# Performance work log

Hardware: AMD Instinct MI355X
Metric: run time of the kernel (lower is better)

The kernel has to match this reference:

```python
import jax, jax.numpy as jnp
import numpy as np

D_MODEL = 1024
NUM_HEADS = 16
D_K = D_MODEL // NUM_HEADS
THETA = 10000.0
BATCH = 2
SEQ = 2048


def apply_rope(x, token_positions):
    # x: [B, H, S, D_K]; token_positions: [S] int
    half = D_K // 2
    inv_freq = THETA ** (-(jnp.arange(half, dtype=jnp.float32) * 2.0) / D_K)  # [half]
    angles = token_positions.astype(jnp.float32)[:, None] * inv_freq[None, :]  # [S, half]
    cos = jnp.cos(angles)  # [S, half]
    sin = jnp.sin(angles)
    x1 = x[..., 0::2]  # even indices
    x2 = x[..., 1::2]  # odd indices
    out_even = x1 * cos - x2 * sin
    out_odd = x1 * sin + x2 * cos
    # interleave back: [..., S, half, 2] -> [..., S, D_K]
    return jnp.stack([out_even, out_odd], axis=-1).reshape(x.shape)


def setup_inputs() -> dict:
    key = jax.random.key(0)
    ks = jax.random.split(key, 5)
    x = jax.random.normal(ks[0], (BATCH, SEQ, D_MODEL), dtype=jnp.float32)
    token_positions = jnp.arange(SEQ, dtype=jnp.int64)
    scale = 0.02
    Wq = jax.random.normal(ks[1], (D_MODEL, D_MODEL), dtype=jnp.float32) * scale
    Wk = jax.random.normal(ks[2], (D_MODEL, D_MODEL), dtype=jnp.float32) * scale
    Wv = jax.random.normal(ks[3], (D_MODEL, D_MODEL), dtype=jnp.float32) * scale
    Wo = jax.random.normal(ks[4], (D_MODEL, D_MODEL), dtype=jnp.float32) * scale
    return {"x": x, "token_positions": token_positions, "Wq": Wq, "Wk": Wk, "Wv": Wv, "Wo": Wo}


def reference(x, token_positions, Wq, Wk, Wv, Wo):
    B, S, _ = x.shape
    # cs336 Linear: y = x @ W.T with W of shape (out, in), no bias
    def proj(W):
        h = jnp.einsum('bsd,od->bso', x, W)
        return h.reshape(B, S, NUM_HEADS, D_K).transpose(0, 2, 1, 3)  # [B,H,S,Dk]
    Q = apply_rope(proj(Wq), token_positions)
    K = apply_rope(proj(Wk), token_positions)
    V = proj(Wv)
    scores = jnp.einsum('bhqd,bhkd->bhqk', Q, K) / jnp.sqrt(jnp.float32(D_K))
    causal = jnp.tril(jnp.ones((S, S), dtype=bool))
    scores = jnp.where(causal, scores, -jnp.inf)
    attn = jax.nn.softmax(scores, axis=-1)
    out = jnp.einsum('bhqk,bhkd->bhqd', attn, V)  # [B,H,S,Dk]
    out = out.transpose(0, 2, 1, 3).reshape(B, S, D_MODEL)
    return jnp.einsum('bsd,od->bso', out, Wo)
```

## Files before the change

kernel.cpp:

```cpp
#include <hip/hip_runtime.h>
#include <hip/hip_bf16.h>
#include <math.h>

#define NHEADS 16
#define DKH 64
#define SEQ 2048
#define DMODEL 1024

typedef __attribute__((ext_vector_type(8))) short short8;
typedef __attribute__((ext_vector_type(4))) float f32x4;

#define GLDS16(g, l)                                         \
  __builtin_amdgcn_global_load_lds(                          \
      (__attribute__((address_space(1))) void*)(void*)(g),   \
      (__attribute__((address_space(3))) void*)(l), 16, 0, 0)

__device__ __forceinline__ short f2bf(float f) {
  unsigned u = __float_as_uint(f);
  unsigned r = (u + 0x7fffu + ((u >> 16) & 1u)) >> 16;
  return (short)r;
}

__device__ __forceinline__ short8 pack8(float4 a, float4 b) {
  short8 v;
  v[0] = f2bf(a.x); v[1] = f2bf(a.y); v[2] = f2bf(a.z); v[3] = f2bf(a.w);
  v[4] = f2bf(b.x); v[5] = f2bf(b.y); v[6] = f2bf(b.z); v[7] = f2bf(b.w);
  return v;
}

__device__ __forceinline__ int swz(int r, int gran) {
  return r * 64 + ((gran ^ (r & 7)) << 3);
}

__global__ __launch_bounds__(256) void precast_rope_kernel(
    const float* __restrict__ X, const float* __restrict__ Wq,
    const float* __restrict__ Wk, const float* __restrict__ Wv,
    const float* __restrict__ Wo, const int* __restrict__ tp,
    short* __restrict__ Xb, short* __restrict__ Wqb, short* __restrict__ Wkb,
    short* __restrict__ Wvb, short* __restrict__ Wob,
    float* __restrict__ ct, float* __restrict__ st) {
  int bid = blockIdx.x;
  if (bid < 4096) {
    int i = bid * 256 + threadIdx.x;
    const float* src; short* dst; int off;
    if (i < 524288) { src = X; dst = Xb; off = i; }
    else {
      int k = i - 524288; int w = k >> 17; off = k & 131071;
      src = (w == 0) ? Wq : (w == 1) ? Wk : (w == 2) ? Wv : Wo;
      dst = (w == 0) ? Wqb : (w == 1) ? Wkb : (w == 2) ? Wvb : Wob;
    }
    const float4* p = reinterpret_cast<const float4*>(src) + 2 * (size_t)off;
    float4 a = p[0], b = p[1];
    reinterpret_cast<short8*>(dst)[off] = pack8(a, b);
  } else {
    int idx = (bid - 4096) * 256 + threadIdx.x;
    if (idx >= SEQ * 32) return;
    int s = idx >> 5, i = idx & 31;
    int is64 = (tp[1] == 0);
    int p = is64 ? tp[2 * s] : tp[s];
    float invf = powf(10000.0f, -(2.0f * (float)i) / 64.0f);
    float a = (float)p * invf;
    ct[idx] = cosf(a);
    st[idx] = sinf(a);
  }
}

__global__ __launch_bounds__(512, 2) void gemm_qkv_kernel(
    const short* __restrict__ X, const short* __restrict__ Wq,
    const short* __restrict__ Wk, const short* __restrict__ Wv,
    short* __restrict__ Qb, short* __restrict__ Kb, short* __restrict__ Vb,
    const float* __restrict__ ct, const float* __restrict__ st) {
  __shared__ __align__(16) short As[2][256 * 64];
  __shared__ __align__(16) short Bs[2][192 * 64];
  const int id = blockIdx.x;
  const int xcd = id & 7, rr = id >> 3;
  const int tm = (xcd & 3) * 4 + (rr & 3);
  const int tn = (xcd >> 2) * 8 + (rr >> 2);
  const int tid = threadIdx.x;
  const int wave = tid >> 6, lane = tid & 63;
  const int l15 = lane & 15, quad = lane >> 4;
  const int wm = wave >> 2, wn = wave & 3;

  const int n0 = tn * 192;
  const short* Abase = X + (size_t)(tm * 256) * DMODEL;
  const short* Bbase = Wq + (size_t)n0 * DMODEL;
  (void)Wk; (void)Wv;

  const int lr = lane >> 3;
  const int lc = (lane & 7) ^ lr;

#define STGA(bufi, half, kt_)                                              \
  do {                                                                     \
    int R0 = (half) * 128 + wave * 16;                                     \
    GLDS16(Abase + (size_t)(R0 + lr) * DMODEL + (kt_) * 64 + lc * 8,       \
           &As[bufi][R0 * 64 + lane * 8]);                                 \
    GLDS16(Abase + (size_t)(R0 + 8 + lr) * DMODEL + (kt_) * 64 + lc * 8,   \
           &As[bufi][(R0 + 8) * 64 + lane * 8]);                           \
  } while (0)
#define STGB(bufi, t, kt_)                                                 \
  do {                                                                     \
    int R0 = (t) * 64 + wave * 8;                                          \
    GLDS16(Bbase + (size_t)(R0 + lr) * DMODEL + (kt_) * 64 + lc * 8,       \
           &Bs[bufi][R0 * 64 + lane * 8]);                                 \
  } while (0)

  f32x4 acc[8][3];
#pragma unroll
  for (int m = 0; m < 8; m++)
#pragma unroll
    for (int n = 0; n < 3; n++) acc[m][n] = (f32x4){0.f, 0.f, 0.f, 0.f};

  STGB(0, 0, 0); STGB(0, 1, 0); STGB(0, 2, 0);
  STGA(0, 0, 0); STGA(0, 1, 0);
  STGB(1, 0, 1); STGB(1, 1, 1); STGB(1, 2, 1);

  short8 bfr[3][2];
  for (int kt = 0; kt < 16; kt++) {
    const int buf = kt & 1;
    if (kt < 15) { STGA(buf ^ 1, 0, kt + 1); }
    if (kt < 15) { asm volatile("s_waitcnt vmcnt(5)" ::: "memory"); }
    else         { asm volatile("s_waitcnt vmcnt(0)" ::: "memory"); }
    asm volatile("s_barrier" ::: "memory");
#pragma unroll
    for (int nb = 0; nb < 3; nb++)
#pragma unroll
      for (int ks = 0; ks < 2; ks++)
        bfr[nb][ks] = *reinterpret_cast<const short8*>(
            &Bs[buf][swz(wn * 48 + nb * 16 + l15, ks * 4 + quad)]);
    {
      short8 af[2][2];
#pragma unroll
      for (int j = 0; j < 2; j++)
#pragma unroll
        for (int ks = 0; ks < 2; ks++)
          af[j][ks] = *reinterpret_cast<const short8*>(
              &As[buf][swz(wm * 128 + j * 16 + l15, ks * 4 + quad)]);
      __builtin_amdgcn_s_setprio(1);
#pragma unroll
      for (int j = 0; j < 2; j++)
#pragma unroll
        for (int nb = 0; nb < 3; nb++)
#pragma unroll
          for (int ks = 0; ks < 2; ks++)
            acc[j][nb] = __builtin_amdgcn_mfma_f32_16x16x32_bf16(
                af[j][ks], bfr[nb][ks], acc[j][nb], 0, 0, 0);
      __builtin_amdgcn_s_setprio(0);
    }
    asm volatile("s_barrier" ::: "memory");
#pragma unroll
    for (int p = 1; p < 4; p++) {
      short8 af[2][2];
#pragma unroll
      for (int j = 0; j < 2; j++)
#pragma unroll
        for (int ks = 0; ks < 2; ks++)
          af[j][ks] = *reinterpret_cast<const short8*>(
              &As[buf][swz(wm * 128 + (p * 2 + j) * 16 + l15, ks * 4 + quad)]);
      if (p == 1)      { if (kt < 15) { STGA(buf ^ 1, 1, kt + 1); } }
      else if (p == 2) { if (kt < 14) { STGB(buf, 0, kt + 2); STGB(buf, 1, kt + 2); } }
      else             { if (kt < 14) { STGB(buf, 2, kt + 2); } }
      asm volatile("s_barrier" ::: "memory");
      __builtin_amdgcn_s_setprio(1);
#pragma unroll
      for (int j = 0; j < 2; j++)
#pragma unroll
        for (int nb = 0; nb < 3; nb++)
#pragma unroll
          for (int ks = 0; ks < 2; ks++)
            acc[p * 2 + j][nb] = __builtin_amdgcn_mfma_f32_16x16x32_bf16(
                af[j][ks], bfr[nb][ks], acc[p * 2 + j][nb], 0, 0, 0);
      __builtin_amdgcn_s_setprio(0);
      asm volatile("s_barrier" ::: "memory");
    }
  }
#undef STGA
#undef STGB

#pragma unroll
  for (int mf = 0; mf < 8; mf++) {
    const int s0g = tm * 256 + wm * 128 + mf * 16 + quad * 4;
    const int b = s0g >> 11, s = s0g & 2047;
#pragma unroll
    for (int nb = 0; nb < 3; nb++) {
      int nl = n0 + wn * 48 + nb * 16 + l15;
      int mid = nl >> 10;
      int c = nl & 1023;
      int h = c >> 6, dd = c & 63;
      if (mid == 2) {
        unsigned u0 = (unsigned)(unsigned short)f2bf(acc[mf][nb][0]) |
                      ((unsigned)(unsigned short)f2bf(acc[mf][nb][1]) << 16);
        unsigned u1 = (unsigned)(unsigned short)f2bf(acc[mf][nb][2]) |
                      ((unsigned)(unsigned short)f2bf(acc[mf][nb][3]) << 16);
        uint2 pk; pk.x = u0; pk.y = u1;
        *reinterpret_cast<uint2*>(Vb + ((size_t)(b * NHEADS + h) * DKH + dd) * SEQ + s) = pk;
      } else {
#pragma unroll
        for (int reg = 0; reg < 4; reg++) {
          float v = acc[mf][nb][reg];
          float pv = __shfl_xor(v, 1);
          int fi = dd >> 1;
          int sg = s + reg;
          float cc = ct[sg * 32 + fi], sn = st[sg * 32 + fi];
          float o = (dd & 1) ? (pv * sn + v * cc) : (v * cc - pv * sn);
          size_t oi = (((size_t)(b * NHEADS + h)) * SEQ + sg) * DKH + dd;
          ((mid == 0) ? Qb : Kb)[oi] = f2bf(o);
        }
      }
    }
  }
}

__global__ __launch_bounds__(256, 4) void attn_kernel(
    const short* __restrict__ Qb, const short* __restrict__ Kb,
    const short* __restrict__ Vtb, short* __restrict__ Ob) {
  __shared__ __align__(16) short QPs[64 * 64];
  __shared__ __align__(16) short Ks[2][64 * 64];
  __shared__ __align__(16) short Vs[2][64 * 64];

  const int id = blockIdx.x;
  const int xx = id & 7;
  const int mm = (((id >> 3) & 3) + (id >> 8)) & 3;
  const int bh = id >> 5;
  const int qt = (mm == 0) ? (31 - xx) : (mm == 1) ? (16 + xx)
               : (mm == 2) ? (15 - xx) : xx;

  const int tid = threadIdx.x;
  const int wave = tid >> 6, lane = tid & 63;
  const int l15 = lane & 15, quad = lane >> 4;
  const int sr0 = tid >> 3, sc = tid & 7;

  const short* Qp = Qb + (size_t)bh * SEQ * DKH;
  const short* Kp = Kb + (size_t)bh * SEQ * DKH;
  const short* Vp = Vtb + (size_t)bh * DKH * SEQ;

  uint4 kreg[2], vreg[2];
#pragma unroll
  for (int i = 0; i < 2; i++) {
    int r = sr0 + i * 32;
    kreg[i] = *reinterpret_cast<const uint4*>(Kp + (size_t)r * DKH + sc * 8);
    vreg[i] = *reinterpret_cast<const uint4*>(Vp + (size_t)r * SEQ + sc * 8);
  }
#pragma unroll
  for (int i = 0; i < 2; i++) {
    int r = sr0 + i * 32;
    uint4 v = *reinterpret_cast<const uint4*>(Qp + (size_t)(qt * 64 + r) * DKH + sc * 8);
    *reinterpret_cast<uint4*>(&QPs[swz(r, sc)]) = v;
  }
#pragma unroll
  for (int i = 0; i < 2; i++) {
    int r = sr0 + i * 32;
    *reinterpret_cast<uint4*>(&Ks[0][swz(r, sc)]) = kreg[i];
    *reinterpret_cast<uint4*>(&Vs[0][swz(r, sc)]) = vreg[i];
  }
  __syncthreads();
  short8 qf0, qf1;
  {
    int r = wave * 16 + l15;
    qf0 = *reinterpret_cast<const short8*>(&QPs[swz(r, quad)]);
    qf1 = *reinterpret_cast<const short8*>(&QPs[swz(r, 4 + quad)]);
  }

  f32x4 accO[4];
#pragma unroll
  for (int i = 0; i < 4; i++) accO[i] = (f32x4){0.f, 0.f, 0.f, 0.f};
  float rs = 0.f;

  const float SCL = 0.125f * 1.44269504089f;
  const float FM = 13.0f;

  int buf = 0;
  for (int kt = 0; kt <= qt; kt++) {
    if (kt < qt) {
#pragma unroll
      for (int i = 0; i < 2; i++) {
        int r = sr0 + i * 32;
        kreg[i] = *reinterpret_cast<const uint4*>(Kp + (size_t)((kt + 1) * 64 + r) * DKH + sc * 8);
        vreg[i] = *reinterpret_cast<const uint4*>(Vp + (size_t)r * SEQ + (kt + 1) * 64 + sc * 8);
      }
    }

    f32x4 sa[4];
#pragma unroll
    for (int nb = 0; nb < 4; nb++) {
      sa[nb] = (f32x4){0.f, 0.f, 0.f, 0.f};
      int r = nb * 16 + l15;
      short8 kf0 = *reinterpret_cast<const short8*>(&Ks[buf][swz(r, quad)]);
      sa[nb] = __builtin_amdgcn_mfma_f32_16x16x32_bf16(kf0, qf0, sa[nb], 0, 0, 0);
      short8 kf1 = *reinterpret_cast<const short8*>(&Ks[buf][swz(r, 4 + quad)]);
      sa[nb] = __builtin_amdgcn_mfma_f32_16x16x32_bf16(kf1, qf1, sa[nb], 0, 0, 0);
    }

    const bool diag = (kt == qt);
    const int prow = wave * 16 + l15;
#pragma unroll
    for (int nb = 0; nb < 4; nb++) {
      float p0 = exp2f(sa[nb][0] * SCL - FM);
      float p1 = exp2f(sa[nb][1] * SCL - FM);
      float p2 = exp2f(sa[nb][2] * SCL - FM);
      float p3 = exp2f(sa[nb][3] * SCL - FM);
      if (diag) {
        int kbase = nb * 16 + quad * 4;
        if (kbase + 0 > prow) p0 = 0.f;
        if (kbase + 1 > prow) p1 = 0.f;
        if (kbase + 2 > prow) p2 = 0.f;
        if (kbase + 3 > prow) p3 = 0.f;
      }
      rs += (p0 + p1) + (p2 + p3);
      unsigned u0 = (unsigned)(unsigned short)f2bf(p0) |
                    ((unsigned)(unsigned short)f2bf(p1) << 16);
      unsigned u1 = (unsigned)(unsigned short)f2bf(p2) |
                    ((unsigned)(unsigned short)f2bf(p3) << 16);
      uint2 pk; pk.x = u0; pk.y = u1;
      int g = 2 * nb + (quad >> 1);
      *reinterpret_cast<uint2*>(&QPs[swz(prow, g) + (quad & 1) * 4]) = pk;
    }

    short8 pf0 = *reinterpret_cast<const short8*>(&QPs[swz(prow, quad)]);
    short8 pf1 = *reinterpret_cast<const short8*>(&QPs[swz(prow, 4 + quad)]);
#pragma unroll
    for (int db = 0; db < 4; db++) {
      int dv = db * 16 + l15;
      short8 vf0 = *reinterpret_cast<const short8*>(&Vs[buf][swz(dv, quad)]);
      accO[db] = __builtin_amdgcn_mfma_f32_16x16x32_bf16(pf0, vf0, accO[db], 0, 0, 0);
      short8 vf1 = *reinterpret_cast<const short8*>(&Vs[buf][swz(dv, 4 + quad)]);
      accO[db] = __builtin_amdgcn_mfma_f32_16x16x32_bf16(pf1, vf1, accO[db], 0, 0, 0);
    }

    if (kt < qt) {
      int nbuf = buf ^ 1;
#pragma unroll
      for (int i = 0; i < 2; i++) {
        int r = sr0 + i * 32;
        *reinterpret_cast<uint4*>(&Ks[nbuf][swz(r, sc)]) = kreg[i];
        *reinterpret_cast<uint4*>(&Vs[nbuf][swz(r, sc)]) = vreg[i];
      }
      __syncthreads();
      buf = nbuf;
    }
  }

  float t = rs;
  t += __shfl_xor(t, 16);
  t += __shfl_xor(t, 32);
  float lv[4];
#pragma unroll
  for (int reg = 0; reg < 4; reg++) lv[reg] = __shfl(t, quad * 4 + reg);

  int b = bh >> 4, h = bh & 15;
#pragma unroll
  for (int db = 0; db < 4; db++)
#pragma unroll
    for (int reg = 0; reg < 4; reg++) {
      int s = qt * 64 + wave * 16 + quad * 4 + reg;
      int dv = db * 16 + l15;
      float o = accO[db][reg] / lv[reg];
      Ob[((size_t)(b * SEQ + s)) * DMODEL + h * DKH + dv] = f2bf(o);
    }
}

__global__ __launch_bounds__(256) void gemm_out_kernel(
    const short* __restrict__ X, const short* __restrict__ Wo, float* __restrict__ Out) {
  __shared__ __align__(16) short As[128 * 64];
  __shared__ __align__(16) short Bs[64 * 64];
  const int tm = blockIdx.x;
  const int tn = blockIdx.y;
  const int tid = threadIdx.x;
  const int wave = tid >> 6, lane = tid & 63;
  const int l15 = lane & 15, quad = lane >> 4;
  const int wm = wave >> 1, wn = wave & 1;

  const short* Abase = X + (size_t)(tm * 128) * DMODEL;
  const short* Bbase = Wo + (size_t)(tn * 64) * DMODEL;

  const int lr = lane >> 3;
  const int lc = (lane & 7) ^ lr;

  f32x4 acc[4][2];
#pragma unroll
  for (int mb = 0; mb < 4; mb++)
#pragma unroll
    for (int nb = 0; nb < 2; nb++) acc[mb][nb] = (f32x4){0.f, 0.f, 0.f, 0.f};

  for (int kk = 0; kk < 16; kk++) {
    const short* Ak = Abase + kk * 64;
    const short* Bk = Bbase + kk * 64;
#pragma unroll
    for (int i = 0; i < 4; i++) {
      int R = i * 32 + wave * 8;
      GLDS16(Ak + (size_t)(R + lr) * DMODEL + lc * 8, &As[R * 64 + lane * 8]);
    }
#pragma unroll
    for (int i = 0; i < 2; i++) {
      int R = i * 32 + wave * 8;
      GLDS16(Bk + (size_t)(R + lr) * DMODEL + lc * 8, &Bs[R * 64 + lane * 8]);
    }
    __syncthreads();
#pragma unroll
    for (int kg = 0; kg < 2; kg++) {
      short8 af[4], bf[2];
#pragma unroll
      for (int mb = 0; mb < 4; mb++) {
        int r = wm * 64 + mb * 16 + l15;
        af[mb] = *reinterpret_cast<const short8*>(&As[swz(r, kg * 4 + quad)]);
      }
#pragma unroll
      for (int nb = 0; nb < 2; nb++) {
        int r = wn * 32 + nb * 16 + l15;
        bf[nb] = *reinterpret_cast<const short8*>(&Bs[swz(r, kg * 4 + quad)]);
      }
#pragma unroll
      for (int mb = 0; mb < 4; mb++)
#pragma unroll
        for (int nb = 0; nb < 2; nb++)
          acc[mb][nb] = __builtin_amdgcn_mfma_f32_16x16x32_bf16(af[mb], bf[nb], acc[mb][nb], 0, 0, 0);
    }
    __syncthreads();
  }
#pragma unroll
  for (int mb = 0; mb < 4; mb++)
#pragma unroll
    for (int nb = 0; nb < 2; nb++)
#pragma unroll
      for (int reg = 0; reg < 4; reg++) {
        int rg = tm * 128 + wm * 64 + mb * 16 + quad * 4 + reg;
        int col = tn * 64 + wn * 32 + nb * 16 + l15;
        Out[(size_t)rg * DMODEL + col] = acc[mb][nb][reg];
      }
}

extern "C" void kernel_launch(void* const* d_in, const int* in_sizes, int n_in,
                              void* d_out, int out_size, void* d_ws, size_t ws_size,
                              hipStream_t stream) {
  (void)in_sizes; (void)n_in; (void)out_size; (void)ws_size;
  const float* X  = (const float*)d_in[0];
  const int*   tp = (const int*)d_in[1];
  const float* Wq = (const float*)d_in[2];
  const float* Wk = (const float*)d_in[3];
  const float* Wv = (const float*)d_in[4];
  const float* Wo = (const float*)d_in[5];
  float* Out = (float*)d_out;

  short* Qb  = (short*)d_ws;
  short* Kb  = Qb + 4194304;
  short* Vb  = Kb + 4194304;
  short* Ab  = Vb + 4194304;
  short* Xb  = Ab + 4194304;
  short* Wqb = Xb + 4194304;
  short* Wkb = Wqb + 1048576;
  short* Wvb = Wkb + 1048576;
  short* Wob = Wvb + 1048576;
  float* ct  = (float*)(Wob + 1048576);
  float* st  = ct + SEQ * 32;

  precast_rope_kernel<<<dim3(4352), dim3(256), 0, stream>>>(
      X, Wq, Wk, Wv, Wo, tp, Xb, Wqb, Wkb, Wvb, Wob, ct, st);
  gemm_qkv_kernel<<<dim3(256), dim3(512), 0, stream>>>(Xb, Wqb, Wkb, Wvb,
                                                       Qb, Kb, Vb, ct, st);
  attn_kernel<<<dim3(1024), dim3(256), 0, stream>>>(Qb, Kb, Vb, Ab);
  gemm_out_kernel<<<dim3(32, 16), dim3(256), 0, stream>>>(Ab, Wob, Out);
}
```

Before: 183.1 us.

## Remap attention blocks, add MFMA priority hints and hardware bf16 packing

Changes the block-to-(batch-head, q-tile) mapping so that consecutive block groups pair short and long causal q-tiles (u and 31-u) and spread batch-heads across XCD-strided ids. This is meant to balance work per CU and improve L2 locality. It also wraps the MFMA sections in s_setprio to favour matrix issue across waves, and replaces the software bf16 rounding with the v_cvt_pk_bf16_f32 instruction. It adds a __syncthreads after the Q fragment read, so later P writes into the shared Q/P buffer cannot race with other waves still reading Q. That barrier fixes a latent hazard at the cost of one extra sync.

```diff
diff --git a/kernel.cpp b/kernel.cpp
--- a/kernel.cpp
+++ b/kernel.cpp
@@ -19,6 +19,12 @@
   unsigned u = __float_as_uint(f);
   unsigned r = (u + 0x7fffu + ((u >> 16) & 1u)) >> 16;
   return (short)r;
+}
+
+__device__ __forceinline__ unsigned cvtpk(float lo, float hi) {
+  unsigned r;
+  asm("v_cvt_pk_bf16_f32 %0, %1, %2" : "=v"(r) : "v"(lo), "v"(hi));
+  return r;
 }
 
 __device__ __forceinline__ short8 pack8(float4 a, float4 b) {
@@ -218,11 +224,11 @@
   __shared__ __align__(16) short Vs[2][64 * 64];
 
   const int id = blockIdx.x;
-  const int xx = id & 7;
-  const int mm = (((id >> 3) & 3) + (id >> 8)) & 3;
-  const int bh = id >> 5;
-  const int qt = (mm == 0) ? (31 - xx) : (mm == 1) ? (16 + xx)
-               : (mm == 2) ? (15 - xx) : xx;
+  const int x8 = id & 7;
+  const int g  = id >> 3;
+  const int bh = x8 * 4 + (g >> 5);
+  const int u  = g & 31;
+  const int qt = (u & 1) ? (31 - (u >> 1)) : (u >> 1);
 
   const int tid = threadIdx.x;
   const int wave = tid >> 6, lane = tid & 63;
@@ -259,6 +265,7 @@
     qf0 = *reinterpret_cast<const short8*>(&QPs[swz(r, quad)]);
     qf1 = *reinterpret_cast<const short8*>(&QPs[swz(r, 4 + quad)]);
   }
+  __syncthreads();
 
   f32x4 accO[4];
 #pragma unroll
@@ -280,6 +287,7 @@
     }
 
     f32x4 sa[4];
+    __builtin_amdgcn_s_setprio(1);
 #pragma unroll
     for (int nb = 0; nb < 4; nb++) {
       sa[nb] = (f32x4){0.f, 0.f, 0.f, 0.f};
@@ -289,6 +297,7 @@
       short8 kf1 = *reinterpret_cast<const short8*>(&Ks[buf][swz(r, 4 + quad)]);
       sa[nb] = __builtin_amdgcn_mfma_f32_16x16x32_bf16(kf1, qf1, sa[nb], 0, 0, 0);
     }
+    __builtin_amdgcn_s_setprio(0);
 
     const bool diag = (kt == qt);
     const int prow = wave * 16 + l15;
@@ -306,17 +315,14 @@
         if (kbase + 3 > prow) p3 = 0.f;
       }
       rs += (p0 + p1) + (p2 + p3);
-      unsigned u0 = (unsigned)(unsigned short)f2bf(p0) |
-                    ((unsigned)(unsigned short)f2bf(p1) << 16);
-      unsigned u1 = (unsigned)(unsigned short)f2bf(p2) |
-                    ((unsigned)(unsigned short)f2bf(p3) << 16);
-      uint2 pk; pk.x = u0; pk.y = u1;
-      int g = 2 * nb + (quad >> 1);
-      *reinterpret_cast<uint2*>(&QPs[swz(prow, g) + (quad & 1) * 4]) = pk;
+      uint2 pk; pk.x = cvtpk(p0, p1); pk.y = cvtpk(p2, p3);
+      int g2 = 2 * nb + (quad >> 1);
+      *reinterpret_cast<uint2*>(&QPs[swz(prow, g2) + (quad & 1) * 4]) = pk;
     }
 
     short8 pf0 = *reinterpret_cast<const short8*>(&QPs[swz(prow, quad)]);
     short8 pf1 = *reinterpret_cast<const short8*>(&QPs[swz(prow, 4 + quad)]);
+    __builtin_amdgcn_s_setprio(1);
 #pragma unroll
     for (int db = 0; db < 4; db++) {
       int dv = db * 16 + l15;
@@ -325,6 +331,7 @@
       short8 vf1 = *reinterpret_cast<const short8*>(&Vs[buf][swz(dv, 4 + quad)]);
       accO[db] = __builtin_amdgcn_mfma_f32_16x16x32_bf16(pf1, vf1, accO[db], 0, 0, 0);
     }
+    __builtin_amdgcn_s_setprio(0);
 
     if (kt < qt) {
       int nbuf = buf ^ 1;
```

New measurement: 198.1 us. 8.2% more time.
